# Kernel tuning notes

Measured on AMD Instinct MI355X. Metric: run time of the kernel, lower is better.

## Reference

```python
import jax, jax.numpy as jnp
import numpy as np

N_NODES = 100000
N_EDGES = 640000
IN_DIM, HID_DIM, OUT_DIM = 128, 64, 32


def setup_inputs() -> dict:
    key = jax.random.key(0)
    ks = jax.random.split(key, 8)
    x = jax.random.normal(ks[0], (N_NODES, IN_DIM), dtype=jnp.float32)
    edge_index = jax.random.randint(ks[1], (2, N_EDGES), 0, N_NODES, dtype=jnp.int64)
    # SAGEConv params: lin_l (applied to aggregated neighbors, has bias),
    # lin_r (applied to root node, no bias) -- PyG defaults.
    s1 = 1.0 / np.sqrt(IN_DIM)
    s2 = 1.0 / np.sqrt(HID_DIM)
    W1l = jax.random.uniform(ks[2], (HID_DIM, IN_DIM), jnp.float32, -s1, s1)
    b1 = jax.random.uniform(ks[3], (HID_DIM,), jnp.float32, -s1, s1)
    W1r = jax.random.uniform(ks[4], (HID_DIM, IN_DIM), jnp.float32, -s1, s1)
    W2l = jax.random.uniform(ks[5], (OUT_DIM, HID_DIM), jnp.float32, -s2, s2)
    b2 = jax.random.uniform(ks[6], (OUT_DIM,), jnp.float32, -s2, s2)
    W2r = jax.random.uniform(ks[7], (OUT_DIM, HID_DIM), jnp.float32, -s2, s2)
    return {"x": x, "edge_index": edge_index,
            "W1l": W1l, "b1": b1, "W1r": W1r,
            "W2l": W2l, "b2": b2, "W2r": W2r}


def _sage_conv(x, src, dst, Wl, b, Wr, num_nodes):
    # mean aggregation of source features onto destination nodes
    msg = x[src]                                                # [E, d]
    agg = jax.ops.segment_sum(msg, dst, num_segments=num_nodes)  # [N, d]
    cnt = jax.ops.segment_sum(jnp.ones((src.shape[0],), x.dtype), dst,
                              num_segments=num_nodes)            # [N]
    agg = agg / jnp.maximum(cnt, 1.0)[:, None]
    # out = lin_l(mean_neighbors) + lin_r(x)
    return agg @ Wl.T + b + x @ Wr.T


def reference(x, edge_index, W1l, b1, W1r, W2l, b2, W2r):
    src, dst = edge_index[0], edge_index[1]
    n = x.shape[0]
    h = jax.nn.relu(_sage_conv(x, src, dst, W1l, b1, W1r, n))
    out = _sage_conv(h, src, dst, W2l, b2, W2r, n)
    return out
```

## Files before the change

kernel.cpp:

```cpp
#include <hip/hip_runtime.h>
#include <hip/hip_bf16.h>

typedef __hip_bfloat16 bf16;
typedef __attribute__((ext_vector_type(8))) short short8;
typedef __attribute__((ext_vector_type(4))) float f32x4;

#define N_NODES 100000
#define N_EDGES 640000
#define NSB 98
#define N_TILES 6250
#define GE 313
#define LIN1_BLKS 1024

__device__ __forceinline__ float bf2f(short s) {
    union { float f; unsigned u; } u;
    u.u = ((unsigned)(unsigned short)s) << 16;
    return u.f;
}
__device__ __forceinline__ short f2s(float f) {
    union { bf16 b; short s; } u;
    u.b = __float2bfloat16(f);
    return u.s;
}

__device__ __forceinline__ int detect_is64(const int* __restrict__ idx) {
    int lane = threadIdx.x & 63;
    int v = idx[2 * (lane & 31) + 1];
    return __ballot(v == 0) == ~0ULL;
}
__device__ __forceinline__ int detect_f32(const unsigned* __restrict__ xw) {
    int lane = threadIdx.x & 63;
    unsigned e = (xw[lane] >> 7) & 0xFFu;
    int inr = (e >= 0x20u && e <= 0x4Fu);
    return __popcll(__ballot(inr)) < 48;
}

__device__ __forceinline__ void decode8(
        const int* __restrict__ eidx, int is64, int e0, int E,
        int (&ss)[8], int (&dd)[8]) {
    if (is64) {
        int4 a0 = *(const int4*)&eidx[2 * e0];
        int4 a1 = *(const int4*)&eidx[2 * e0 + 4];
        int4 a2 = *(const int4*)&eidx[2 * e0 + 8];
        int4 a3 = *(const int4*)&eidx[2 * e0 + 12];
        int4 b0 = *(const int4*)&eidx[2 * (E + e0)];
        int4 b1 = *(const int4*)&eidx[2 * (E + e0) + 4];
        int4 b2 = *(const int4*)&eidx[2 * (E + e0) + 8];
        int4 b3 = *(const int4*)&eidx[2 * (E + e0) + 12];
        ss[0] = a0.x; ss[1] = a0.z; ss[2] = a1.x; ss[3] = a1.z;
        ss[4] = a2.x; ss[5] = a2.z; ss[6] = a3.x; ss[7] = a3.z;
        dd[0] = b0.x; dd[1] = b0.z; dd[2] = b1.x; dd[3] = b1.z;
        dd[4] = b2.x; dd[5] = b2.z; dd[6] = b3.x; dd[7] = b3.z;
    } else {
        int4 s0 = *(const int4*)&eidx[e0];
        int4 s1 = *(const int4*)&eidx[e0 + 4];
        int4 d0 = *(const int4*)&eidx[E + e0];
        int4 d1 = *(const int4*)&eidx[E + e0 + 4];
        ss[0] = s0.x; ss[1] = s0.y; ss[2] = s0.z; ss[3] = s0.w;
        ss[4] = s1.x; ss[5] = s1.y; ss[6] = s1.z; ss[7] = s1.w;
        dd[0] = d0.x; dd[1] = d0.y; dd[2] = d0.z; dd[3] = d0.w;
        dd[4] = d1.x; dd[5] = d1.y; dd[6] = d1.z; dd[7] = d1.w;
    }
}

__device__ __forceinline__ short8 load_frag(const void* base, size_t eoff, int f32) {
    if (f32) {
        const float4* p = (const float4*)((const float*)base + eoff);
        const float4 u = p[0], v = p[1];
        short8 r;
        r[0] = f2s(u.x); r[1] = f2s(u.y); r[2] = f2s(u.z); r[3] = f2s(u.w);
        r[4] = f2s(v.x); r[5] = f2s(v.y); r[6] = f2s(v.z); r[7] = f2s(v.w);
        return r;
    }
    return *(const short8*)((const short*)base + eoff);
}

__global__ __launch_bounds__(256) void lin1_hist_kernel(
        const void* __restrict__ x, const void* __restrict__ W1l,
        const void* __restrict__ W1r, bf16* __restrict__ xl,
        bf16* __restrict__ xr, const int* __restrict__ eidx,
        int* __restrict__ deg, int* __restrict__ rank) {
    __shared__ short wlds[2][16][64][8];
    const int tid = threadIdx.x;

    if (blockIdx.x >= LIN1_BLKS) {
        const int blk = blockIdx.x - LIN1_BLKS;
        const int is64 = detect_is64(eidx);
        int e0 = (blk * 256 + tid) * 8;
        if (e0 >= N_EDGES) return;
        int ss[8], dd[8], rk[8];
        decode8(eidx, is64, e0, N_EDGES, ss, dd);
#pragma unroll
        for (int c = 0; c < 8; ++c) {
            bool ok = (unsigned)ss[c] < (unsigned)N_NODES &&
                      (unsigned)dd[c] < (unsigned)N_NODES;
            rk[c] = ok ? atomicAdd(&deg[dd[c]], 1) : 0;
        }
        *(int4*)&rank[e0]     = make_int4(rk[0], rk[1], rk[2], rk[3]);
        *(int4*)&rank[e0 + 4] = make_int4(rk[4], rk[5], rk[6], rk[7]);
        return;
    }

    const int f32 = detect_f32((const unsigned*)x);
    {
        const int l = tid & 63, fg = tid >> 6;
        const int mm = l & 15, qq = l >> 4;
#pragma unroll
        for (int i = 0; i < 4; ++i) {
            const int f = fg * 4 + i;
            const int ks = f >> 2, dt = f & 3;
            const size_t wo = (size_t)(dt * 16 + mm) * 128 + ks * 32 + qq * 8;
            *(short8*)&wlds[0][f][l][0] = load_frag(W1l, wo, f32);
            *(short8*)&wlds[1][f][l][0] = load_frag(W1r, wo, f32);
        }
    }
    __syncthreads();

    const int nwaves = LIN1_BLKS * 4;
    const int wid = blockIdx.x * 4 + (tid >> 6);
    const int lane = tid & 63;
    const int m = lane & 15, quad = lane >> 4;
    const short* wl0 = &wlds[0][0][lane][0];
    const short* wr0 = &wlds[1][0][lane][0];

    int tile = wid;
    if (tile >= N_TILES) return;

    short8 a[4];
    {
        const size_t arow = (size_t)(tile * 16 + m) * 128 + quad * 8;
#pragma unroll
        for (int ks = 0; ks < 4; ++ks)
            a[ks] = load_frag(x, arow + ks * 32, f32);
    }

    while (true) {
        const int nxt = tile + nwaves;
        short8 an[4];
        if (nxt < N_TILES) {
            const size_t arow = (size_t)(nxt * 16 + m) * 128 + quad * 8;
#pragma unroll
            for (int ks = 0; ks < 4; ++ks)
                an[ks] = load_frag(x, arow + ks * 32, f32);
        }

        f32x4 accl[4], accr[4];
#pragma unroll
        for (int dt = 0; dt < 4; ++dt) {
            accl[dt] = (f32x4){0.f, 0.f, 0.f, 0.f};
            accr[dt] = (f32x4){0.f, 0.f, 0.f, 0.f};
        }
#pragma unroll
        for (int ks = 0; ks < 4; ++ks)
#pragma unroll
            for (int dt = 0; dt < 4; ++dt) {
                const short8 wl = *(const short8*)(wl0 + (ks * 4 + dt) * 512);
                const short8 wr = *(const short8*)(wr0 + (ks * 4 + dt) * 512);
                accl[dt] = __builtin_amdgcn_mfma_f32_16x16x32_bf16(
                    wl, a[ks], accl[dt], 0, 0, 0);
                accr[dt] = __builtin_amdgcn_mfma_f32_16x16x32_bf16(
                    wr, a[ks], accr[dt], 0, 0, 0);
            }

        const int node = tile * 16 + m;
#pragma unroll
        for (int dt = 0; dt < 4; ++dt) {
            short4 pl, pr;
            pl.x = f2s(accl[dt][0]); pl.y = f2s(accl[dt][1]);
            pl.z = f2s(accl[dt][2]); pl.w = f2s(accl[dt][3]);
            pr.x = f2s(accr[dt][0]); pr.y = f2s(accr[dt][1]);
            pr.z = f2s(accr[dt][2]); pr.w = f2s(accr[dt][3]);
            *(short4*)((short*)xl + (size_t)node * 64 + dt * 16 + quad * 4) = pl;
            *(short4*)((short*)xr + (size_t)node * 64 + dt * 16 + quad * 4) = pr;
        }

        if (nxt >= N_TILES) break;
        tile = nxt;
#pragma unroll
        for (int ks = 0; ks < 4; ++ks) a[ks] = an[ks];
    }
}

__global__ __launch_bounds__(256) void scan_partial_kernel(
        const int* __restrict__ deg, int* __restrict__ off,
        int* __restrict__ bsum, int N) {
    __shared__ int ss[256];
    const int tid = threadIdx.x, blk = blockIdx.x;
    const int base = blk * 1024 + tid * 4;
    int v[4], s = 0;
    if (base + 3 < N) {
        int4 dv = *(const int4*)&deg[base];
        v[0] = dv.x; v[1] = dv.y; v[2] = dv.z; v[3] = dv.w;
    } else {
#pragma unroll
        for (int c = 0; c < 4; ++c) v[c] = (base + c < N) ? deg[base + c] : 0;
    }
#pragma unroll
    for (int c = 0; c < 4; ++c) s += v[c];
    ss[tid] = s; __syncthreads();
    for (int o = 1; o < 256; o <<= 1) {
        int t = (tid >= o) ? ss[tid - o] : 0;
        __syncthreads();
        ss[tid] += t;
        __syncthreads();
    }
    int run = ss[tid] - s;
    if (tid == 255) bsum[blk] = ss[255];
#pragma unroll
    for (int c = 0; c < 4; ++c) {
        if (base + c < N) off[base + c] = run;
        run += v[c];
    }
}

__global__ __launch_bounds__(256) void scan_add_kernel(
        int* __restrict__ off, const int* __restrict__ bsum, int N) {
    __shared__ int ss[NSB];
    const int blk = blockIdx.x, tid = threadIdx.x;
    if (tid < NSB) ss[tid] = bsum[tid];
    __syncthreads();
    int add = 0;
    for (int i = 0; i < blk; ++i) add += ss[i];
    const int base = blk * 1024 + tid * 4;
#pragma unroll
    for (int c = 0; c < 4; ++c) {
        int i = base + c;
        if (i < N) off[i] += add;
    }
    if (blk == NSB - 1 && tid == 0)
        off[N] = add + ss[NSB - 1];
}

__global__ __launch_bounds__(256) void fill_kernel(
        const int* __restrict__ eidx, const int* __restrict__ off,
        const int* __restrict__ rank, int* __restrict__ srcs, int E, int N) {
    const int is64 = detect_is64(eidx);
    int e0 = (blockIdx.x * 256 + threadIdx.x) * 8;
    if (e0 >= E) return;
    int ss[8], dd[8];
    decode8(eidx, is64, e0, E, ss, dd);
    int4 r0 = *(const int4*)&rank[e0];
    int4 r1 = *(const int4*)&rank[e0 + 4];
    const int rk[8] = {r0.x, r0.y, r0.z, r0.w, r1.x, r1.y, r1.z, r1.w};
#pragma unroll
    for (int c = 0; c < 8; ++c) {
        if ((unsigned)ss[c] >= (unsigned)N || (unsigned)dd[c] >= (unsigned)N) continue;
        srcs[off[dd[c]] + rk[c]] = ss[c];
    }
}

__global__ __launch_bounds__(256) void gather1_lin2_kernel(
        const int* __restrict__ srcs, const int* __restrict__ off,
        const bf16* __restrict__ xl, const bf16* __restrict__ xr,
        const void* __restrict__ b1, const void* __restrict__ W2l,
        const void* __restrict__ W2r, bf16* __restrict__ hl,
        bf16* __restrict__ hr, const unsigned* __restrict__ xdet) {
    const int f32 = detect_f32(xdet);
    const int tid = threadIdx.x;
    const int lane = tid & 63, wave = tid >> 6;
    const int m = lane & 15, quad = lane >> 4;

    const void* Wb = (wave < 2) ? W2l : W2r;
    short8 bfrag[2];
#pragma unroll
    for (int ks = 0; ks < 2; ++ks)
        bfrag[ks] = load_frag(
            Wb, (size_t)((wave & 1) * 16 + m) * 64 + ks * 32 + quad * 8, f32);

    __shared__ short htile[16][72];

    const int node = blockIdx.x * 16 + (tid >> 4);
    const int j = tid & 15;
    const int gbase = lane & ~15;
    const int a = off[node], b = off[node + 1];
    float a0 = 0.f, a1 = 0.f, a2 = 0.f, a3 = 0.f;
    for (int base = a; base < b; base += 16) {
        const int cdeg = min(b - base, 16);
        int sv = (j < cdeg) ? srcs[base + j] : 0;
        for (int bb = 0; bb < cdeg; bb += 4) {
#pragma unroll
            for (int t = 0; t < 4; ++t) {
                const int idx = bb + t;
                const int s = __shfl(sv, gbase + (idx < cdeg ? idx : 0));
                if (idx < cdeg) {
                    short4 v = *(const short4*)((const short*)xl + (size_t)s * 64 + j * 4);
                    a0 += bf2f(v.x); a1 += bf2f(v.y);
                    a2 += bf2f(v.z); a3 += bf2f(v.w);
                }
            }
        }
    }
    float b0, b1v, b2v, b3;
    if (f32) {
        float4 bb4 = *(const float4*)((const float*)b1 + j * 4);
        b0 = bb4.x; b1v = bb4.y; b2v = bb4.z; b3 = bb4.w;
    } else {
        short4 bb4 = *(const short4*)((const short*)b1 + j * 4);
        b0 = bf2f(bb4.x); b1v = bf2f(bb4.y); b2v = bf2f(bb4.z); b3 = bf2f(bb4.w);
    }
    short4 xr4 = *(const short4*)((const short*)xr + (size_t)node * 64 + j * 4);
    const float inv = 1.0f / fmaxf((float)(b - a), 1.0f);
    short4 o;
    o.x = f2s(fmaxf(a0 * inv + b0  + bf2f(xr4.x), 0.0f));
    o.y = f2s(fmaxf(a1 * inv + b1v + bf2f(xr4.y), 0.0f));
    o.z = f2s(fmaxf(a2 * inv + b2v + bf2f(xr4.z), 0.0f));
    o.w = f2s(fmaxf(a3 * inv + b3  + bf2f(xr4.w), 0.0f));
    *(short4*)&htile[tid >> 4][j * 4] = o;
    __syncthreads();

    short8 afr[2];
#pragma unroll
    for (int ks = 0; ks < 2; ++ks)
        afr[ks] = *(const short8*)&htile[m][ks * 32 + quad * 8];
    f32x4 acc = (f32x4){0.f, 0.f, 0.f, 0.f};
#pragma unroll
    for (int ks = 0; ks < 2; ++ks)
        acc = __builtin_amdgcn_mfma_f32_16x16x32_bf16(
            bfrag[ks], afr[ks], acc, 0, 0, 0);

    bf16* dst = (wave < 2) ? hl : hr;
    const int onode = blockIdx.x * 16 + m;
    short4 p;
    p.x = f2s(acc[0]); p.y = f2s(acc[1]);
    p.z = f2s(acc[2]); p.w = f2s(acc[3]);
    *(short4*)((short*)dst + (size_t)onode * 32 + (wave & 1) * 16 + quad * 4) = p;
}

__global__ __launch_bounds__(256) void gather2_kernel(
        const int* __restrict__ srcs, const int* __restrict__ off,
        const bf16* __restrict__ hl, const bf16* __restrict__ hr,
        const void* __restrict__ b2, void* __restrict__ out,
        const unsigned* __restrict__ xdet, int N) {
    const int f32 = detect_f32(xdet);
    const int tid = threadIdx.x;
    const int node = blockIdx.x * 32 + (tid >> 3);
    const int j = tid & 7;
    const int gbase = (tid & 63) & ~7;
    const int a = off[node], b = off[node + 1];
    float a0 = 0.f, a1 = 0.f, a2 = 0.f, a3 = 0.f;
    for (int base = a; base < b; base += 8) {
        const int cdeg = min(b - base, 8);
        int sv = (j < cdeg) ? srcs[base + j] : 0;
        for (int bb = 0; bb < cdeg; bb += 4) {
#pragma unroll
            for (int t = 0; t < 4; ++t) {
                const int idx = bb + t;
                const int s = __shfl(sv, gbase + (idx < cdeg ? idx : 0));
                if (idx < cdeg) {
                    short4 v = *(const short4*)((const short*)hl + (size_t)s * 32 + j * 4);
                    a0 += bf2f(v.x); a1 += bf2f(v.y);
                    a2 += bf2f(v.z); a3 += bf2f(v.w);
                }
            }
        }
    }
    float b0, b1v, b2v, b3;
    if (f32) {
        float4 bb4 = *(const float4*)((const float*)b2 + j * 4);
        b0 = bb4.x; b1v = bb4.y; b2v = bb4.z; b3 = bb4.w;
    } else {
        short4 bb4 = *(const short4*)((const short*)b2 + j * 4);
        b0 = bf2f(bb4.x); b1v = bf2f(bb4.y); b2v = bf2f(bb4.z); b3 = bf2f(bb4.w);
    }
    short4 hr4 = *(const short4*)((const short*)hr + (size_t)node * 32 + j * 4);
    const float inv = 1.0f / fmaxf((float)(b - a), 1.0f);
    const float v0 = a0 * inv + b0  + bf2f(hr4.x);
    const float v1 = a1 * inv + b1v + bf2f(hr4.y);
    const float v2 = a2 * inv + b2v + bf2f(hr4.z);
    const float v3 = a3 * inv + b3  + bf2f(hr4.w);
    if (f32) {
        *(float4*)((float*)out + (size_t)node * 32 + j * 4) =
            make_float4(v0, v1, v2, v3);
    } else {
        short4 o;
        o.x = f2s(v0); o.y = f2s(v1); o.z = f2s(v2); o.w = f2s(v3);
        *(short4*)((short*)out + (size_t)node * 32 + j * 4) = o;
    }
}

extern "C" void kernel_launch(void* const* d_in, const int* in_sizes, int n_in,
                              void* d_out, int out_size, void* d_ws, size_t ws_size,
                              hipStream_t stream) {
    const void* x   = d_in[0];
    const int*  eix = (const int*)d_in[1];
    const void* W1l = d_in[2];
    const void* b1  = d_in[3];
    const void* W1r = d_in[4];
    const void* W2l = d_in[5];
    const void* b2  = d_in[6];
    const void* W2r = d_in[7];

    const int N = N_NODES;
    const int E = N_EDGES;

    char* ws = (char*)d_ws;
    bf16*  xl    = (bf16*)(ws + 256);
    bf16*  xr    = (bf16*)(ws + 256 + (size_t)N * 128);
    bf16*  hl    = (bf16*)(ws + 256 + (size_t)N * 384);
    bf16*  hr    = (bf16*)(ws + 256 + (size_t)N * 448);
    int*   off   = (int*) (ws + 256 + (size_t)N * 512);
    int*   deg   = off + (N + 4);
    int*   rank  = deg + N;
    int*   srcs  = rank + E;
    int*   bsum  = srcs + E;

    hipMemsetAsync(deg, 0, (size_t)N * 4, stream);

    lin1_hist_kernel<<<LIN1_BLKS + GE, 256, 0, stream>>>(
        x, W1l, W1r, xl, xr, eix, deg, rank);

    scan_partial_kernel<<<NSB, 256, 0, stream>>>(deg, off, bsum, N);
    scan_add_kernel<<<NSB, 256, 0, stream>>>(off, bsum, N);
    fill_kernel<<<GE, 256, 0, stream>>>(eix, off, rank, srcs, E, N);

    gather1_lin2_kernel<<<N / 16, 256, 0, stream>>>(
        srcs, off, xl, xr, b1, W2l, W2r, hl, hr, (const unsigned*)x);

    gather2_kernel<<<N / 32, 256, 0, stream>>>(
        srcs, off, hl, hr, b2, d_out, (const unsigned*)x, N);
}
```

Before: 212.8 us.

## Split histogram from lin1 kernel and batch gather loads for more memory parallelism

Splits the fused lin1+histogram kernel into a standalone histogram kernel (4 edges per thread, 625 blocks) and a separate lin1 kernel launched after the scan/fill stages. The two gather kernels now issue up to 8 neighbor-row loads into registers before accumulating, so more loads are in flight at once. The split drops the overlap between the atomic histogram and the dense GEMM and adds one kernel launch. The batched loads raise register use and do extra zero-padded iterations for low-degree nodes.

```diff
diff --git a/kernel.cpp b/kernel.cpp
--- a/kernel.cpp
+++ b/kernel.cpp
@@ -10,6 +10,7 @@
 #define NSB 98
 #define N_TILES 6250
 #define GE 313
+#define HB 625
 #define LIN1_BLKS 1024
 
 __device__ __forceinline__ float bf2f(short s) {
@@ -63,6 +64,40 @@
     }
 }
 
+__device__ __forceinline__ void decode4(
+        const int* __restrict__ eidx, int is64, int e0, int E,
+        int (&ss)[4], int (&dd)[4]) {
+    if (is64) {
+        int4 a0 = *(const int4*)&eidx[2 * e0];
+        int4 a1 = *(const int4*)&eidx[2 * e0 + 4];
+        int4 b0 = *(const int4*)&eidx[2 * (E + e0)];
+        int4 b1 = *(const int4*)&eidx[2 * (E + e0) + 4];
+        ss[0] = a0.x; ss[1] = a0.z; ss[2] = a1.x; ss[3] = a1.z;
+        dd[0] = b0.x; dd[1] = b0.z; dd[2] = b1.x; dd[3] = b1.z;
+    } else {
+        int4 s0 = *(const int4*)&eidx[e0];
+        int4 d0 = *(const int4*)&eidx[E + e0];
+        ss[0] = s0.x; ss[1] = s0.y; ss[2] = s0.z; ss[3] = s0.w;
+        dd[0] = d0.x; dd[1] = d0.y; dd[2] = d0.z; dd[3] = d0.w;
+    }
+}
+
+__global__ __launch_bounds__(256) void hist_kernel(
+        const int* __restrict__ eidx, int* __restrict__ deg,
+        int* __restrict__ rank) {
+    const int is64 = detect_is64(eidx);
+    const int e0 = (blockIdx.x * 256 + threadIdx.x) * 4;
+    int ss[4], dd[4], rk[4];
+    decode4(eidx, is64, e0, N_EDGES, ss, dd);
+#pragma unroll
+    for (int c = 0; c < 4; ++c) {
+        bool ok = (unsigned)ss[c] < (unsigned)N_NODES &&
+                  (unsigned)dd[c] < (unsigned)N_NODES;
+        rk[c] = ok ? atomicAdd(&deg[dd[c]], 1) : 0;
+    }
+    *(int4*)&rank[e0] = make_int4(rk[0], rk[1], rk[2], rk[3]);
+}
+
 __device__ __forceinline__ short8 load_frag(const void* base, size_t eoff, int f32) {
     if (f32) {
         const float4* p = (const float4*)((const float*)base + eoff);
@@ -75,33 +110,14 @@
     return *(const short8*)((const short*)base + eoff);
 }
 
-__global__ __launch_bounds__(256) void lin1_hist_kernel(
+__global__ __launch_bounds__(256) void lin1_kernel(
         const void* __restrict__ x, const void* __restrict__ W1l,
         const void* __restrict__ W1r, bf16* __restrict__ xl,
-        bf16* __restrict__ xr, const int* __restrict__ eidx,
-        int* __restrict__ deg, int* __restrict__ rank) {
+        bf16* __restrict__ xr) {
+    const int f32 = detect_f32((const unsigned*)x);
     __shared__ short wlds[2][16][64][8];
+
     const int tid = threadIdx.x;
-
-    if (blockIdx.x >= LIN1_BLKS) {
-        const int blk = blockIdx.x - LIN1_BLKS;
-        const int is64 = detect_is64(eidx);
-        int e0 = (blk * 256 + tid) * 8;
-        if (e0 >= N_EDGES) return;
-        int ss[8], dd[8], rk[8];
-        decode8(eidx, is64, e0, N_EDGES, ss, dd);
-#pragma unroll
-        for (int c = 0; c < 8; ++c) {
-            bool ok = (unsigned)ss[c] < (unsigned)N_NODES &&
-                      (unsigned)dd[c] < (unsigned)N_NODES;
-            rk[c] = ok ? atomicAdd(&deg[dd[c]], 1) : 0;
-        }
-        *(int4*)&rank[e0]     = make_int4(rk[0], rk[1], rk[2], rk[3]);
-        *(int4*)&rank[e0 + 4] = make_int4(rk[4], rk[5], rk[6], rk[7]);
-        return;
-    }
-
-    const int f32 = detect_f32((const unsigned*)x);
     {
         const int l = tid & 63, fg = tid >> 6;
         const int mm = l & 15, qq = l >> 4;
@@ -277,16 +293,21 @@
     for (int base = a; base < b; base += 16) {
         const int cdeg = min(b - base, 16);
         int sv = (j < cdeg) ? srcs[base + j] : 0;
-        for (int bb = 0; bb < cdeg; bb += 4) {
-#pragma unroll
-            for (int t = 0; t < 4; ++t) {
+        for (int bb = 0; bb < cdeg; bb += 8) {
+            short4 v[8];
+#pragma unroll
+            for (int t = 0; t < 8; ++t) {
                 const int idx = bb + t;
                 const int s = __shfl(sv, gbase + (idx < cdeg ? idx : 0));
-                if (idx < cdeg) {
-                    short4 v = *(const short4*)((const short*)xl + (size_t)s * 64 + j * 4);
-                    a0 += bf2f(v.x); a1 += bf2f(v.y);
-                    a2 += bf2f(v.z); a3 += bf2f(v.w);
-                }
+                if (idx < cdeg)
+                    v[t] = *(const short4*)((const short*)xl + (size_t)s * 64 + j * 4);
+                else
+                    v[t] = make_short4(0, 0, 0, 0);
+            }
+#pragma unroll
+            for (int t = 0; t < 8; ++t) {
+                a0 += bf2f(v[t].x); a1 += bf2f(v[t].y);
+                a2 += bf2f(v[t].z); a3 += bf2f(v[t].w);
             }
         }
     }
@@ -341,17 +362,19 @@
     for (int base = a; base < b; base += 8) {
         const int cdeg = min(b - base, 8);
         int sv = (j < cdeg) ? srcs[base + j] : 0;
-        for (int bb = 0; bb < cdeg; bb += 4) {
-#pragma unroll
-            for (int t = 0; t < 4; ++t) {
-                const int idx = bb + t;
-                const int s = __shfl(sv, gbase + (idx < cdeg ? idx : 0));
-                if (idx < cdeg) {
-                    short4 v = *(const short4*)((const short*)hl + (size_t)s * 32 + j * 4);
-                    a0 += bf2f(v.x); a1 += bf2f(v.y);
-                    a2 += bf2f(v.z); a3 += bf2f(v.w);
-                }
-            }
+        short4 v[8];
+#pragma unroll
+        for (int t = 0; t < 8; ++t) {
+            const int s = __shfl(sv, gbase + (t < cdeg ? t : 0));
+            if (t < cdeg)
+                v[t] = *(const short4*)((const short*)hl + (size_t)s * 32 + j * 4);
+            else
+                v[t] = make_short4(0, 0, 0, 0);
+        }
+#pragma unroll
+        for (int t = 0; t < 8; ++t) {
+            a0 += bf2f(v[t].x); a1 += bf2f(v[t].y);
+            a2 += bf2f(v[t].z); a3 += bf2f(v[t].w);
         }
     }
     float b0, b1v, b2v, b3;
@@ -406,13 +429,14 @@
 
     hipMemsetAsync(deg, 0, (size_t)N * 4, stream);
 
-    lin1_hist_kernel<<<LIN1_BLKS + GE, 256, 0, stream>>>(
-        x, W1l, W1r, xl, xr, eix, deg, rank);
+    hist_kernel<<<HB, 256, 0, stream>>>(eix, deg, rank);
 
     scan_partial_kernel<<<NSB, 256, 0, stream>>>(deg, off, bsum, N);
     scan_add_kernel<<<NSB, 256, 0, stream>>>(off, bsum, N);
     fill_kernel<<<GE, 256, 0, stream>>>(eix, off, rank, srcs, E, N);
 
+    lin1_kernel<<<LIN1_BLKS, 256, 0, stream>>>(x, W1l, W1r, xl, xr);
+
     gather1_lin2_kernel<<<N / 16, 256, 0, stream>>>(
         srcs, off, xl, xr, b1, W2l, W2r, hl, hr, (const unsigned*)x);
 
```

New measurement: 208.0 us. 2.3% less time.
